# Optimization experiments

Hardware: AMD Instinct MI355X
Metric: run time of the kernel (lower is better)

The kernel has to match this reference:

```python
import jax, jax.numpy as jnp
import numpy as np

EPS = 1e-5
KERNELS = [3, 3, 5, 7]  # 2*i+1 for i>=1, first layer k=3


def _conv_relu_bn(x, w, b, gamma, beta, rmean, rvar):
    # x: [B, Cin, S], w: [Cout, Cin, K]
    k = w.shape[-1]
    y = jax.lax.conv_general_dilated(
        x, w, window_strides=(1,), padding=[(k // 2, k // 2)],
        dimension_numbers=("NCW", "OIW", "NCW"))
    y = y + b[None, :, None]
    y = jax.nn.relu(y)
    # BatchNorm1d in inference mode (running stats)
    inv = gamma[None, :, None] / jnp.sqrt(rvar[None, :, None] + EPS)
    return (y - rmean[None, :, None]) * inv + beta[None, :, None]


def setup_inputs() -> dict:
    key = jax.random.key(0)
    ks = jax.random.split(key, 32)
    B, S = 128, 8192
    inp = {"x": jax.random.normal(ks[0], (B, 4, S), dtype=jnp.float32)}
    cin = 4
    for i, k in enumerate(KERNELS):
        inp[f"w{i}"] = jax.random.normal(ks[1 + i], (32, cin, k), dtype=jnp.float32) * 0.1
        inp[f"b{i}"] = jnp.zeros((32,), jnp.float32)
        inp[f"g{i}"] = jnp.ones((32,), jnp.float32)   # BN gamma
        inp[f"bb{i}"] = jnp.zeros((32,), jnp.float32)  # BN beta
        inp[f"rm{i}"] = jnp.zeros((32,), jnp.float32)  # running mean
        inp[f"rv{i}"] = jnp.ones((32,), jnp.float32)   # running var
        cin = 32
    inp["fw1"] = jax.random.normal(ks[10], (16, 32), dtype=jnp.float32) * 0.1
    inp["fb1"] = jnp.zeros((16,), jnp.float32)
    inp["fw2"] = jax.random.normal(ks[11], (1, 16), dtype=jnp.float32) * 0.1
    inp["fb2"] = jnp.zeros((1,), jnp.float32)
    return inp


def reference(x,
              w0, b0, g0, bb0, rm0, rv0,
              w1, b1, g1, bb1, rm1, rv1,
              w2, b2, g2, bb2, rm2, rv2,
              w3, b3, g3, bb3, rm3, rv3,
              fw1, fb1, fw2, fb2):
    x = _conv_relu_bn(x, w0, b0, g0, bb0, rm0, rv0)
    x = _conv_relu_bn(x, w1, b1, g1, bb1, rm1, rv1)
    x = _conv_relu_bn(x, w2, b2, g2, bb2, rm2, rv2)
    x = _conv_relu_bn(x, w3, b3, g3, bb3, rm3, rv3)
    # [B, 32, S] -> [B, S, 32]; the original per-timestep MLP loop is one batched GEMM
    h = jnp.einsum("bcs,hc->bsh", x, fw1) + fb1
    h = jax.nn.relu(h)  # Dropout(0.1) is identity in eval
    out = jnp.einsum("bsh,oh->bso", h, fw2) + fb2
    return out[..., 0]  # squeeze(-1) -> [B, S]
```

## Files before the change

### kernel.cpp

```cpp
#include <hip/hip_runtime.h>

#define SEQ    8192
#define S_TILE 180
#define POSN   192
#define NROW   198
#define CS     1608
#define NTHR   256
#define NREC   37
#define BN_HALFOFF (NREC*512)

typedef __attribute__((ext_vector_type(8))) _Float16 half8;
typedef __attribute__((ext_vector_type(4))) _Float16 half4v;
typedef __attribute__((ext_vector_type(4))) float    f32x4;

__device__ __forceinline__ int uni(int v){ return __builtin_amdgcn_readfirstlane(v); }

extern "C" __global__ void prep_kernel(
    const float* w0, const float* w1, const float* w2, const float* w3,
    const float* b0, const float* g0, const float* bb0, const float* rm0, const float* rv0,
    const float* b1, const float* g1, const float* bb1, const float* rm1, const float* rv1,
    const float* b2, const float* g2, const float* bb2, const float* rm2, const float* rv2,
    const float* b3, const float* g3, const float* bb3, const float* rm3, const float* rv3,
    const float* fw1, _Float16* ws)
{
    const int tid  = threadIdx.x;
    const int rec  = blockIdx.x;
    if (rec < NREC) {
        if (tid < 64) {
            const int lane = tid;
            const float* W; int CIN, K, r2;
            if      (rec < 6)  { W = w0;  CIN = 4;  K = 3; r2 = rec;      }
            else if (rec < 12) { W = w1;  CIN = 32; K = 3; r2 = rec - 6;  }
            else if (rec < 22) { W = w2;  CIN = 32; K = 5; r2 = rec - 12; }
            else if (rec < 36) { W = w3;  CIN = 32; K = 7; r2 = rec - 22; }
            else               { W = fw1; CIN = 32; K = 1; r2 = 0;        }
            int tap = r2 >> 1, mh = r2 & 1;
            int co  = mh*16 + (lane & 15);
            int ci0 = (lane >> 4) * 8;
            half8 h;
#pragma unroll
            for (int j = 0; j < 8; ++j) {
                int ci = ci0 + j;
                h[j] = (_Float16)((ci < CIN) ? W[(co*CIN + ci)*K + tap] : 0.0f);
            }
            *(half8*)(ws + rec*512 + lane*8) = h;
        }
    } else if (tid < 128) {
        int l = tid >> 5, co = tid & 31;
        const float *g, *bb, *rm, *rv, *bi;
        if      (l == 0) { g=g0; bb=bb0; rm=rm0; rv=rv0; bi=b0; }
        else if (l == 1) { g=g1; bb=bb1; rm=rm1; rv=rv1; bi=b1; }
        else if (l == 2) { g=g2; bb=bb2; rm=rm2; rv=rv2; bi=b2; }
        else             { g=g3; bb=bb3; rm=rm3; rv=rv3; bi=b3; }
        float scale = g[co] / sqrtf(rv[co] + 1e-5f);
        float shift = bb[co] - rm[co]*scale;
        float* bn = (float*)(ws + BN_HALFOFF) + (l*32 + co)*4;
        bn[0] = scale; bn[1] = shift; bn[2] = bi[co]; bn[3] = 0.0f;
    }
}

template<int K, int DOFF, bool BC0>
__device__ __forceinline__ void conv_layer(
    const _Float16* __restrict__ rec, const float4* __restrict__ bn,
    const _Float16* in, _Float16* outb, int s0, int ntb, int lane)
{
    const int q = lane >> 4, n = lane & 15;
    const _Float16* bbase = in + (BC0 ? 0 : q*CS) + (ntb*16 + n)*8;

    f32x4 acc[3][2];
#pragma unroll
    for (int nt = 0; nt < 3; ++nt)
#pragma unroll
        for (int mh = 0; mh < 2; ++mh) acc[nt][mh] = (f32x4){0.f, 0.f, 0.f, 0.f};

#pragma unroll
    for (int tap = 0; tap < K; ++tap) {
        half8 a0 = *(const half8*)(rec + (tap*2 + 0)*512 + lane*8);
        half8 a1 = *(const half8*)(rec + (tap*2 + 1)*512 + lane*8);
#pragma unroll
        for (int nt = 0; nt < 3; ++nt) {
            half8 bf = *(const half8*)(bbase + nt*128 + tap*8);
            acc[nt][0] = __builtin_amdgcn_mfma_f32_16x16x32_f16(a0, bf, acc[nt][0], 0, 0, 0);
            acc[nt][1] = __builtin_amdgcn_mfma_f32_16x16x32_f16(a1, bf, acc[nt][1], 0, 0, 0);
        }
    }

#pragma unroll
    for (int nt = 0; nt < 3; ++nt) {
        int pos = (ntb + nt)*16 + n;
        bool oob = (unsigned)(s0 + DOFF + pos) >= SEQ;
#pragma unroll
        for (int mh = 0; mh < 2; ++mh) {
            int co0 = mh*16 + q*4;
            half4v hv;
#pragma unroll
            for (int r = 0; r < 4; ++r) {
                float4 p = bn[co0 + r];
                float v = fmaxf(acc[nt][mh][r] + p.z, 0.0f)*p.x + p.y;
                if (oob) v = 0.0f;
                hv[r] = (_Float16)v;
            }
            int cb = mh*2 + (q >> 1);
            *(half4v*)(outb + cb*CS + pos*8 + (q & 1)*4) = hv;
        }
    }
}

extern "C" __global__ void __launch_bounds__(NTHR, 6)
dnashape_mfma(const float* __restrict__ x, const _Float16* __restrict__ ws,
              const float* __restrict__ fb1, const float* __restrict__ fw2,
              const float* __restrict__ fb2, float* __restrict__ out)
{
    __shared__ _Float16 bufA[4*CS];
    __shared__ _Float16 bufB[4*CS];

    const int tid  = threadIdx.x;
    const int tile = blockIdx.x, b = blockIdx.y;
    const int s0   = tile * S_TILE;

    for (int li = tid; li < NROW; li += NTHR) {
        int sg = s0 - 7 + li;
        bool ok = (unsigned)sg < SEQ;
        float v0 = ok ? x[(b*4 + 0)*SEQ + sg] : 0.f;
        float v1 = ok ? x[(b*4 + 1)*SEQ + sg] : 0.f;
        float v2 = ok ? x[(b*4 + 2)*SEQ + sg] : 0.f;
        float v3 = ok ? x[(b*4 + 3)*SEQ + sg] : 0.f;
        half8 h0 = {(_Float16)v0, (_Float16)v1, (_Float16)v2, (_Float16)v3, 0, 0, 0, 0};
        *(half8*)(bufB + 0*CS + li*8) = h0;
    }
    const half8 z8 = {0,0,0,0,0,0,0,0};
    if (tid < 32) *(half8*)(bufA + (tid >> 3)*CS + (192 + (tid & 7))*8) = z8;
    __syncthreads();

    const int lane = tid & 63;
    const int ntb  = uni(tid >> 6) * 3;
    const float4* bn = (const float4*)(ws + BN_HALFOFF);

    conv_layer<3, -6, true >(ws +  0*512, bn +  0, bufB, bufA, s0, ntb, lane);
    __syncthreads();
    conv_layer<3, -5, false>(ws +  6*512, bn + 32, bufA, bufB, s0, ntb, lane);
    __syncthreads();
    conv_layer<5, -3, false>(ws + 12*512, bn + 64, bufB, bufA, s0, ntb, lane);
    __syncthreads();
    conv_layer<7,  0, false>(ws + 22*512, bn + 96, bufA, bufB, s0, ntb, lane);
    __syncthreads();

    {
        const int q = lane >> 4, n = lane & 15;
        half8 am = *(const half8*)(ws + 36*512 + lane*8);
        float fb1v[4], fw2v[4];
#pragma unroll
        for (int r = 0; r < 4; ++r) { fb1v[r] = fb1[q*4 + r]; fw2v[r] = fw2[q*4 + r]; }
        float fb2v = fb2[0];
#pragma unroll
        for (int nt = 0; nt < 3; ++nt) {
            int pos = (ntb + nt)*16 + n;
            half8 bf = *(const half8*)(bufB + q*CS + pos*8);
            f32x4 d = {0.f, 0.f, 0.f, 0.f};
            d = __builtin_amdgcn_mfma_f32_16x16x32_f16(am, bf, d, 0, 0, 0);
            float part = 0.f;
#pragma unroll
            for (int r = 0; r < 4; ++r) part += fmaxf(d[r] + fb1v[r], 0.f)*fw2v[r];
            part += __shfl_xor(part, 16, 64);
            part += __shfl_xor(part, 32, 64);
            if (lane < 16) {
                int g = s0 + pos;
                if (pos < S_TILE && g < SEQ) out[b*SEQ + g] = part + fb2v;
            }
        }
    }
}

extern "C" void kernel_launch(void* const* d_in, const int* in_sizes, int n_in,
                              void* d_out, int out_size, void* d_ws, size_t ws_size,
                              hipStream_t stream) {
    const float* p[29];
    for (int i = 0; i < 29; ++i) p[i] = (const float*)d_in[i];
    _Float16* ws = (_Float16*)d_ws;

    prep_kernel<<<dim3(NREC + 1), 128, 0, stream>>>(
        p[1], p[7], p[13], p[19],
        p[2], p[3], p[4], p[5], p[6],
        p[8], p[9], p[10], p[11], p[12],
        p[14], p[15], p[16], p[17], p[18],
        p[20], p[21], p[22], p[23], p[24],
        p[25], ws);

    dim3 grid((SEQ + S_TILE - 1) / S_TILE, 128);
    dnashape_mfma<<<grid, NTHR, 0, stream>>>(p[0], (const _Float16*)ws,
                                             p[26], p[27], p[28], (float*)d_out);
}
```

Measured before the change: 178.9 us.

## Fold BatchNorm into next-layer weights and process two images per block

Each layer's BatchNorm scale is folded into the next layer's fp16 weights, and its shift into the next layer's bias and the FC1 bias, all in the prep kernel. The conv epilogue becomes just a bias add and ReLU, with padded positions filled with -t/s so they equal zero after the implicit BN. The main kernel also moves to 512 threads handling two batch images per block, halving the grid and sharing the weight loads. The risks are extra register pressure under the 512-thread launch bound, and precision loss when the scaled weights or -t/s values are stored in fp16.

Result: slower. 190.3 us (+6.4%).

```diff
diff --git a/kernel.cpp b/kernel.cpp
--- a/kernel.cpp
+++ b/kernel.cpp
@@ -2,10 +2,9 @@
 
 #define SEQ    8192
 #define S_TILE 180
-#define POSN   192
 #define NROW   198
 #define CS     1608
-#define NTHR   256
+#define NTHR   512
 #define NREC   37
 #define BN_HALFOFF (NREC*512)
 
@@ -21,19 +20,19 @@
     const float* b1, const float* g1, const float* bb1, const float* rm1, const float* rv1,
     const float* b2, const float* g2, const float* bb2, const float* rm2, const float* rv2,
     const float* b3, const float* g3, const float* bb3, const float* rm3, const float* rv3,
-    const float* fw1, _Float16* ws)
+    const float* fw1, const float* fb1, _Float16* ws)
 {
-    const int tid  = threadIdx.x;
-    const int rec  = blockIdx.x;
+    const int tid = threadIdx.x;
+    const int rec = blockIdx.x;
     if (rec < NREC) {
         if (tid < 64) {
             const int lane = tid;
-            const float* W; int CIN, K, r2;
+            const float* W; const float *gp = nullptr, *rvp = nullptr; int CIN, K, r2;
             if      (rec < 6)  { W = w0;  CIN = 4;  K = 3; r2 = rec;      }
-            else if (rec < 12) { W = w1;  CIN = 32; K = 3; r2 = rec - 6;  }
-            else if (rec < 22) { W = w2;  CIN = 32; K = 5; r2 = rec - 12; }
-            else if (rec < 36) { W = w3;  CIN = 32; K = 7; r2 = rec - 22; }
-            else               { W = fw1; CIN = 32; K = 1; r2 = 0;        }
+            else if (rec < 12) { W = w1;  CIN = 32; K = 3; r2 = rec - 6;  gp = g0; rvp = rv0; }
+            else if (rec < 22) { W = w2;  CIN = 32; K = 5; r2 = rec - 12; gp = g1; rvp = rv1; }
+            else if (rec < 36) { W = w3;  CIN = 32; K = 7; r2 = rec - 22; gp = g2; rvp = rv2; }
+            else               { W = fw1; CIN = 32; K = 1; r2 = 0;        gp = g3; rvp = rv3; }
             int tap = r2 >> 1, mh = r2 & 1;
             int co  = mh*16 + (lane & 15);
             int ci0 = (lane >> 4) * 8;
@@ -41,27 +40,52 @@
 #pragma unroll
             for (int j = 0; j < 8; ++j) {
                 int ci = ci0 + j;
-                h[j] = (_Float16)((ci < CIN) ? W[(co*CIN + ci)*K + tap] : 0.0f);
+                float wv = (ci < CIN) ? W[(co*CIN + ci)*K + tap] : 0.0f;
+                if (gp) wv *= gp[ci & 31] * rsqrtf(rvp[ci & 31] + 1e-5f);
+                h[j] = (_Float16)wv;
             }
             *(half8*)(ws + rec*512 + lane*8) = h;
         }
-    } else if (tid < 128) {
-        int l = tid >> 5, co = tid & 31;
-        const float *g, *bb, *rm, *rv, *bi;
-        if      (l == 0) { g=g0; bb=bb0; rm=rm0; rv=rv0; bi=b0; }
-        else if (l == 1) { g=g1; bb=bb1; rm=rm1; rv=rv1; bi=b1; }
-        else if (l == 2) { g=g2; bb=bb2; rm=rm2; rv=rv2; bi=b2; }
-        else             { g=g3; bb=bb3; rm=rm3; rv=rv3; bi=b3; }
-        float scale = g[co] / sqrtf(rv[co] + 1e-5f);
-        float shift = bb[co] - rm[co]*scale;
-        float* bn = (float*)(ws + BN_HALFOFF) + (l*32 + co)*4;
-        bn[0] = scale; bn[1] = shift; bn[2] = bi[co]; bn[3] = 0.0f;
+    } else {
+        float* fa = (float*)(ws + BN_HALFOFF);
+        if (tid < 128) {
+            int l = tid >> 5, co = tid & 31;
+            const float *g, *bb, *rm, *rv, *bi, *W = nullptr;
+            const float *gp, *bbp, *rmp, *rvp; int K = 0;
+            if      (l == 0) { g=g0; bb=bb0; rm=rm0; rv=rv0; bi=b0; gp=bbp=rmp=rvp=nullptr; }
+            else if (l == 1) { g=g1; bb=bb1; rm=rm1; rv=rv1; bi=b1; W=w1; K=3; gp=g0; bbp=bb0; rmp=rm0; rvp=rv0; }
+            else if (l == 2) { g=g2; bb=bb2; rm=rm2; rv=rv2; bi=b2; W=w2; K=5; gp=g1; bbp=bb1; rmp=rm1; rvp=rv1; }
+            else             { g=g3; bb=bb3; rm=rm3; rv=rv3; bi=b3; W=w3; K=7; gp=g2; bbp=bb2; rmp=rm2; rvp=rv2; }
+            float s = g[co] * rsqrtf(rv[co] + 1e-5f);
+            float t = bb[co] - rm[co]*s;
+            float bias = bi[co];
+            if (l > 0) {
+                for (int ci = 0; ci < 32; ++ci) {
+                    float sp = gp[ci] * rsqrtf(rvp[ci] + 1e-5f);
+                    float tp = bbp[ci] - rmp[ci]*sp;
+                    float wsum = 0.f;
+                    for (int tap = 0; tap < K; ++tap) wsum += W[(co*32 + ci)*K + tap];
+                    bias += wsum * tp;
+                }
+            }
+            fa[(l*32 + co)*2 + 0] = bias;
+            fa[(l*32 + co)*2 + 1] = -t / s;
+        } else if (tid < 144) {
+            int hh = tid - 128;
+            float acc = fb1[hh];
+            for (int c = 0; c < 32; ++c) {
+                float s3 = g3[c] * rsqrtf(rv3[c] + 1e-5f);
+                float t3 = bb3[c] - rm3[c]*s3;
+                acc += fw1[hh*32 + c] * t3;
+            }
+            fa[256 + hh] = acc;
+        }
     }
 }
 
 template<int K, int DOFF, bool BC0>
 __device__ __forceinline__ void conv_layer(
-    const _Float16* __restrict__ rec, const float4* __restrict__ bn,
+    const _Float16* __restrict__ rec, const float2* __restrict__ bo,
     const _Float16* in, _Float16* outb, int s0, int ntb, int lane)
 {
     const int q = lane >> 4, n = lane & 15;
@@ -95,9 +119,9 @@
             half4v hv;
 #pragma unroll
             for (int r = 0; r < 4; ++r) {
-                float4 p = bn[co0 + r];
-                float v = fmaxf(acc[nt][mh][r] + p.z, 0.0f)*p.x + p.y;
-                if (oob) v = 0.0f;
+                float2 p = bo[co0 + r];
+                float v = fmaxf(acc[nt][mh][r] + p.x, 0.0f);
+                if (oob) v = p.y;
                 hv[r] = (_Float16)v;
             }
             int cb = mh*2 + (q >> 1);
@@ -108,41 +132,50 @@
 
 extern "C" __global__ void __launch_bounds__(NTHR, 6)
 dnashape_mfma(const float* __restrict__ x, const _Float16* __restrict__ ws,
-              const float* __restrict__ fb1, const float* __restrict__ fw2,
-              const float* __restrict__ fb2, float* __restrict__ out)
+              const float* __restrict__ fw2, const float* __restrict__ fb2,
+              float* __restrict__ out)
 {
-    __shared__ _Float16 bufA[4*CS];
-    __shared__ _Float16 bufB[4*CS];
+    __shared__ _Float16 bufA[2][4*CS];
+    __shared__ _Float16 bufB[2][4*CS];
 
     const int tid  = threadIdx.x;
-    const int tile = blockIdx.x, b = blockIdx.y;
+    const int tile = blockIdx.x;
     const int s0   = tile * S_TILE;
-
-    for (int li = tid; li < NROW; li += NTHR) {
-        int sg = s0 - 7 + li;
-        bool ok = (unsigned)sg < SEQ;
-        float v0 = ok ? x[(b*4 + 0)*SEQ + sg] : 0.f;
-        float v1 = ok ? x[(b*4 + 1)*SEQ + sg] : 0.f;
-        float v2 = ok ? x[(b*4 + 2)*SEQ + sg] : 0.f;
-        float v3 = ok ? x[(b*4 + 3)*SEQ + sg] : 0.f;
-        half8 h0 = {(_Float16)v0, (_Float16)v1, (_Float16)v2, (_Float16)v3, 0, 0, 0, 0};
-        *(half8*)(bufB + 0*CS + li*8) = h0;
-    }
-    const half8 z8 = {0,0,0,0,0,0,0,0};
-    if (tid < 32) *(half8*)(bufA + (tid >> 3)*CS + (192 + (tid & 7))*8) = z8;
+    const int b0i  = blockIdx.y * 2;
+
+    const int timg = tid >> 8;
+    {
+        const float* xb = x + (b0i + timg)*4*SEQ;
+        for (int li = (tid & 255); li < NROW; li += 256) {
+            int sg = s0 - 7 + li;
+            bool ok = (unsigned)sg < SEQ;
+            float v0 = ok ? xb[0*SEQ + sg] : 0.f;
+            float v1 = ok ? xb[1*SEQ + sg] : 0.f;
+            float v2 = ok ? xb[2*SEQ + sg] : 0.f;
+            float v3 = ok ? xb[3*SEQ + sg] : 0.f;
+            half8 h0 = {(_Float16)v0, (_Float16)v1, (_Float16)v2, (_Float16)v3, 0, 0, 0, 0};
+            *(half8*)(&bufB[timg][0*CS + li*8]) = h0;
+        }
+        const half8 z8 = {0,0,0,0,0,0,0,0};
+        int u = tid & 255;
+        if (u < 32) *(half8*)(&bufA[timg][(u >> 3)*CS + (192 + (u & 7))*8]) = z8;
+    }
     __syncthreads();
 
     const int lane = tid & 63;
-    const int ntb  = uni(tid >> 6) * 3;
-    const float4* bn = (const float4*)(ws + BN_HALFOFF);
-
-    conv_layer<3, -6, true >(ws +  0*512, bn +  0, bufB, bufA, s0, ntb, lane);
-    __syncthreads();
-    conv_layer<3, -5, false>(ws +  6*512, bn + 32, bufA, bufB, s0, ntb, lane);
-    __syncthreads();
-    conv_layer<5, -3, false>(ws + 12*512, bn + 64, bufB, bufA, s0, ntb, lane);
-    __syncthreads();
-    conv_layer<7,  0, false>(ws + 22*512, bn + 96, bufA, bufB, s0, ntb, lane);
+    const int wv   = uni(tid >> 6);
+    const int img  = wv >> 2;
+    const int ntb  = (wv & 3) * 3;
+    const float*  fa = (const float*)(ws + BN_HALFOFF);
+    const float2* bo = (const float2*)fa;
+
+    conv_layer<3, -6, true >(ws +  0*512, bo +  0, bufB[img], bufA[img], s0, ntb, lane);
+    __syncthreads();
+    conv_layer<3, -5, false>(ws +  6*512, bo + 32, bufA[img], bufB[img], s0, ntb, lane);
+    __syncthreads();
+    conv_layer<5, -3, false>(ws + 12*512, bo + 64, bufB[img], bufA[img], s0, ntb, lane);
+    __syncthreads();
+    conv_layer<7,  0, false>(ws + 22*512, bo + 96, bufA[img], bufB[img], s0, ntb, lane);
     __syncthreads();
 
     {
@@ -150,12 +183,13 @@
         half8 am = *(const half8*)(ws + 36*512 + lane*8);
         float fb1v[4], fw2v[4];
 #pragma unroll
-        for (int r = 0; r < 4; ++r) { fb1v[r] = fb1[q*4 + r]; fw2v[r] = fw2[q*4 + r]; }
+        for (int r = 0; r < 4; ++r) { fb1v[r] = fa[256 + q*4 + r]; fw2v[r] = fw2[q*4 + r]; }
         float fb2v = fb2[0];
+        const int b = b0i + img;
 #pragma unroll
         for (int nt = 0; nt < 3; ++nt) {
             int pos = (ntb + nt)*16 + n;
-            half8 bf = *(const half8*)(bufB + q*CS + pos*8);
+            half8 bf = *(const half8*)(&bufB[img][q*CS + pos*8]);
             f32x4 d = {0.f, 0.f, 0.f, 0.f};
             d = __builtin_amdgcn_mfma_f32_16x16x32_f16(am, bf, d, 0, 0, 0);
             float part = 0.f;
@@ -178,15 +212,15 @@
     for (int i = 0; i < 29; ++i) p[i] = (const float*)d_in[i];
     _Float16* ws = (_Float16*)d_ws;
 
-    prep_kernel<<<dim3(NREC + 1), 128, 0, stream>>>(
+    prep_kernel<<<dim3(NREC + 1), 144, 0, stream>>>(
         p[1], p[7], p[13], p[19],
         p[2], p[3], p[4], p[5], p[6],
         p[8], p[9], p[10], p[11], p[12],
         p[14], p[15], p[16], p[17], p[18],
         p[20], p[21], p[22], p[23], p[24],
-        p[25], ws);
-
-    dim3 grid((SEQ + S_TILE - 1) / S_TILE, 128);
+        p[25], p[26], ws);
+
+    dim3 grid((SEQ + S_TILE - 1) / S_TILE, 64);
     dnashape_mfma<<<grid, NTHR, 0, stream>>>(p[0], (const _Float16*)ws,
-                                             p[26], p[27], p[28], (float*)d_out);
-}
+                                             p[27], p[28], (float*)d_out);
+}
```
